# Kernel optimization log

Measured on AMD Instinct MI355X. Metric: run time of the kernel, lower is better.

## Reference

```python
import jax, jax.numpy as jnp
import numpy as np

N = 50000
E = 800000
D_IN = 128
D_HID = 128
D_OUT = 64


def setup_inputs() -> dict:
    key = jax.random.key(0)
    ks = jax.random.split(key, 9)
    x = jax.random.normal(ks[0], (N, D_IN), dtype=jnp.float32)
    edge_index = jax.random.randint(ks[1], (2, E), 0, N, dtype=jnp.int64)
    # PyG SAGEConv params: lin_l (neighbor path, with bias), lin_r (root path, no bias)
    s1 = 1.0 / np.sqrt(D_IN)
    s2 = 1.0 / np.sqrt(D_HID)
    return {
        "x": x,
        "edge_index": edge_index,
        "W1l": jax.random.uniform(ks[2], (D_IN, D_HID), jnp.float32, -s1, s1),
        "b1": jax.random.uniform(ks[3], (D_HID,), jnp.float32, -s1, s1),
        "W1r": jax.random.uniform(ks[4], (D_IN, D_HID), jnp.float32, -s1, s1),
        "W2l": jax.random.uniform(ks[5], (D_HID, D_OUT), jnp.float32, -s2, s2),
        "b2": jax.random.uniform(ks[6], (D_OUT,), jnp.float32, -s2, s2),
        "W2r": jax.random.uniform(ks[7], (D_HID, D_OUT), jnp.float32, -s2, s2),
    }


def _sage_conv(h, src, dst, Wl, b, Wr, n_nodes):
    # mean-aggregate source features onto target nodes
    msg = h[src]  # [E, d] gather
    summed = jax.ops.segment_sum(msg, dst, num_segments=n_nodes)
    cnt = jax.ops.segment_sum(jnp.ones((src.shape[0],), h.dtype), dst, num_segments=n_nodes)
    mean = summed / jnp.maximum(cnt, 1.0)[:, None]
    return mean @ Wl + b + h @ Wr


def reference(x, edge_index, W1l, b1, W1r, W2l, b2, W2r):
    src, dst = edge_index[0], edge_index[1]
    n = x.shape[0]
    h = jax.nn.relu(_sage_conv(x, src, dst, W1l, b1, W1r, n))
    # dropout is identity in eval mode
    return _sage_conv(h, src, dst, W2l, b2, W2r, n)
```

## Files before the change

kernel.cpp:

```cpp
#include <hip/hip_runtime.h>

#define NN   50000
#define NE   800000
#define CAP  48
#define NPG  6250
#define EPB  3125
#define SEG  576

#define BIN_BLOCKS  256
#define CVT_BLOCKS  (3125 + 128)
#define ZERO_BLOCKS 196
#define SCAT_BLOCKS 2048

typedef __attribute__((ext_vector_type(8))) short bf16x8;
typedef __attribute__((ext_vector_type(4))) unsigned short u16x4;
typedef __attribute__((ext_vector_type(4))) float f32x4;

__device__ __forceinline__ unsigned short f2b(float f) {
    unsigned int u = __builtin_bit_cast(unsigned int, f);
    u += 0x7FFFu + ((u >> 16) & 1u);
    return (unsigned short)(u >> 16);
}
__device__ __forceinline__ float b2f_lo(unsigned int u) {
    return __builtin_bit_cast(float, u << 16);
}
__device__ __forceinline__ float b2f_hi(unsigned int u) {
    return __builtin_bit_cast(float, u & 0xFFFF0000u);
}

__global__ __launch_bounds__(256) void prep_kernel(const int* __restrict__ src,
                                                   const int* __restrict__ dst,
                                                   int* __restrict__ bcnt,
                                                   unsigned* __restrict__ stage,
                                                   const float* __restrict__ x,
                                                   const float* __restrict__ W1l,
                                                   const float* __restrict__ W1r,
                                                   const float* __restrict__ W2l,
                                                   const float* __restrict__ W2r,
                                                   unsigned short* __restrict__ xb,
                                                   unsigned short* __restrict__ Bt1,
                                                   unsigned short* __restrict__ Bt2,
                                                   int* __restrict__ cursor) {
    if (blockIdx.x < BIN_BLOCKS) {
        __shared__ int cnt[16][8];
        __shared__ int repoff[16][8];
        const int tid = threadIdx.x;
        const int b   = blockIdx.x;
        const int r   = tid >> 4;
        if (tid < 128) ((int*)cnt)[tid] = 0;
        __syncthreads();

        unsigned recs[13], metas[13];
#pragma unroll
        for (int it = 0; it < 13; ++it) {
            const int i = it * 256 + tid;
            metas[it] = 0xFFFFFFFFu;
            if (i < EPB) {
                const int e = b * EPB + i;
                const int s = src[e], d = dst[e];
                const int g = d / NPG;
                const int dloc = d - g * NPG;
                const int slot = atomicAdd(&cnt[r][g], 1);
                recs[it]  = ((unsigned)dloc << 16) | (unsigned)s;
                metas[it] = ((unsigned)r << 20) | ((unsigned)g << 16) | (unsigned)slot;
            }
        }
        __syncthreads();
        if (tid < 8) {
            int off = 0;
#pragma unroll
            for (int rr = 0; rr < 16; ++rr) { repoff[rr][tid] = off; off += cnt[rr][tid]; }
            bcnt[tid * 256 + b] = off;
        }
        __syncthreads();
#pragma unroll
        for (int it = 0; it < 13; ++it) {
            if (metas[it] != 0xFFFFFFFFu) {
                const int rr   = metas[it] >> 20;
                const int g    = (metas[it] >> 16) & 7;
                const int slot = metas[it] & 0xFFFF;
                const int pos  = repoff[rr][g] + slot;
                if (pos < SEG) stage[((g << 8) + b) * SEG + pos] = recs[it];
            }
        }
    } else if (blockIdx.x < BIN_BLOCKS + 3125) {
        int i = (blockIdx.x - BIN_BLOCKS) * 256 + threadIdx.x;
        const float4* p = reinterpret_cast<const float4*>(x) + (size_t)i * 2;
        float4 a = p[0], b = p[1];
        uint4 u;
        u.x = (unsigned)f2b(a.x) | ((unsigned)f2b(a.y) << 16);
        u.y = (unsigned)f2b(a.z) | ((unsigned)f2b(a.w) << 16);
        u.z = (unsigned)f2b(b.x) | ((unsigned)f2b(b.y) << 16);
        u.w = (unsigned)f2b(b.z) | ((unsigned)f2b(b.w) << 16);
        reinterpret_cast<uint4*>(xb)[i] = u;
    } else if (blockIdx.x < BIN_BLOCKS + CVT_BLOCKS) {
        int t = (blockIdx.x - BIN_BLOCKS - 3125) * 256 + threadIdx.x;
        if (t < 32768) {
            int c = t >> 8, k = t & 255;
            float v = (k < 128) ? W1l[k * 128 + c] : W1r[(k - 128) * 128 + c];
            Bt1[c * 256 + k] = f2b(v);
        }
        if (t < 16384) {
            int c = t >> 7, k = t & 127;
            float v = (c < 64) ? W2l[k * 64 + c] : W2r[k * 64 + (c - 64)];
            Bt2[c * 128 + k] = f2b(v);
        }
    } else {
        int i = (blockIdx.x - BIN_BLOCKS - CVT_BLOCKS) * 256 + threadIdx.x;
        if (i < NN) cursor[i] = 0;
    }
}

__global__ __launch_bounds__(256) void scatter_kernel(const int* __restrict__ bcnt,
                                                      const unsigned* __restrict__ stage,
                                                      int* __restrict__ cursor,
                                                      unsigned short* __restrict__ col) {
    const int g = blockIdx.x & 7;
    const int b = blockIdx.x >> 3;
    int cnt = bcnt[g * 256 + b];
    if (cnt > SEG) cnt = SEG;
    const unsigned* sp = stage + (size_t)((g << 8) + b) * SEG;
    const int n0 = g * NPG;
    for (int i = threadIdx.x; i < cnt; i += 256) {
        unsigned rec = sp[i];
        int d = n0 + (int)(rec >> 16);
        int p = atomicAdd(&cursor[d], 1);
        if (p < CAP) col[d * CAP + p] = (unsigned short)(rec & 0xFFFFu);
    }
}

__global__ __launch_bounds__(256) void agg_gemm12(const unsigned short* __restrict__ xb,
                                                  const int* __restrict__ cursor,
                                                  const unsigned short* __restrict__ col,
                                                  const unsigned short* __restrict__ Bt1,
                                                  const unsigned short* __restrict__ Bt2,
                                                  const float* __restrict__ b1,
                                                  unsigned short* __restrict__ hlb,
                                                  unsigned short* __restrict__ hrb) {
    constexpr int LDA = 264;
    constexpr int LDH = 136;
    __shared__ unsigned short As[64 * LDA];

    const int base = blockIdx.x * 64;
    const int tid  = threadIdx.x;
    const int l    = tid & 15;
    const int sub  = tid >> 4;

    const uint4* fp = reinterpret_cast<const uint4*>(xb);

    for (int gq = 0; gq < 4; ++gq) {
        const int r  = gq * 16 + sub;
        const int gn = base + r;
        float a0 = 0.f, a1 = 0.f, a2 = 0.f, a3 = 0.f,
              a4 = 0.f, a5 = 0.f, a6 = 0.f, a7 = 0.f;
        uint4 xrow = make_uint4(0, 0, 0, 0);
        if (gn < NN) {
            int len = cursor[gn];
            len = (len > CAP) ? CAP : len;
            const unsigned short* cl = col + gn * CAP;
            int j = 0;
            for (; j + 4 <= len; j += 4) {
                u16x4 c4 = *reinterpret_cast<const u16x4*>(cl + j);
                uint4 v0 = fp[(int)c4[0] * 16 + l];
                uint4 v1 = fp[(int)c4[1] * 16 + l];
                uint4 v2 = fp[(int)c4[2] * 16 + l];
                uint4 v3 = fp[(int)c4[3] * 16 + l];
                a0 += (b2f_lo(v0.x) + b2f_lo(v1.x)) + (b2f_lo(v2.x) + b2f_lo(v3.x));
                a1 += (b2f_hi(v0.x) + b2f_hi(v1.x)) + (b2f_hi(v2.x) + b2f_hi(v3.x));
                a2 += (b2f_lo(v0.y) + b2f_lo(v1.y)) + (b2f_lo(v2.y) + b2f_lo(v3.y));
                a3 += (b2f_hi(v0.y) + b2f_hi(v1.y)) + (b2f_hi(v2.y) + b2f_hi(v3.y));
                a4 += (b2f_lo(v0.z) + b2f_lo(v1.z)) + (b2f_lo(v2.z) + b2f_lo(v3.z));
                a5 += (b2f_hi(v0.z) + b2f_hi(v1.z)) + (b2f_hi(v2.z) + b2f_hi(v3.z));
                a6 += (b2f_lo(v0.w) + b2f_lo(v1.w)) + (b2f_lo(v2.w) + b2f_lo(v3.w));
                a7 += (b2f_hi(v0.w) + b2f_hi(v1.w)) + (b2f_hi(v2.w) + b2f_hi(v3.w));
            }
            for (; j < len; ++j) {
                uint4 v0 = fp[(int)cl[j] * 16 + l];
                a0 += b2f_lo(v0.x);  a1 += b2f_hi(v0.x);
                a2 += b2f_lo(v0.y);  a3 += b2f_hi(v0.y);
                a4 += b2f_lo(v0.z);  a5 += b2f_hi(v0.z);
                a6 += b2f_lo(v0.w);  a7 += b2f_hi(v0.w);
            }
            const float inv = 1.0f / fmaxf((float)len, 1.0f);
            a0 *= inv; a1 *= inv; a2 *= inv; a3 *= inv;
            a4 *= inv; a5 *= inv; a6 *= inv; a7 *= inv;
            xrow = fp[gn * 16 + l];
        }
        uint4 u;
        u.x = (unsigned)f2b(a0) | ((unsigned)f2b(a1) << 16);
        u.y = (unsigned)f2b(a2) | ((unsigned)f2b(a3) << 16);
        u.z = (unsigned)f2b(a4) | ((unsigned)f2b(a5) << 16);
        u.w = (unsigned)f2b(a6) | ((unsigned)f2b(a7) << 16);
        *reinterpret_cast<uint4*>(&As[r * LDA + l * 8])       = u;
        *reinterpret_cast<uint4*>(&As[r * LDA + 128 + l * 8]) = xrow;
    }
    __syncthreads();

    const int wid  = tid >> 6, lane = tid & 63;
    const int lr   = lane & 15;
    const int lk   = (lane >> 4) * 8;
    const int ccol = lane & 15;
    const int ri   = (lane >> 4) * 4;

    f32x4 acc[4][2];
#pragma unroll
    for (int t = 0; t < 4; ++t) {
        acc[t][0] = (f32x4){0.f, 0.f, 0.f, 0.f};
        acc[t][1] = (f32x4){0.f, 0.f, 0.f, 0.f};
    }
    for (int ks = 0; ks < 8; ++ks) {
        const int k = ks * 32 + lk;
        bf16x8 b0 = *reinterpret_cast<const bf16x8*>(Bt1 + (size_t)(wid * 32 + lr) * 256 + k);
        bf16x8 b1 = *reinterpret_cast<const bf16x8*>(Bt1 + (size_t)(wid * 32 + 16 + lr) * 256 + k);
#pragma unroll
        for (int t = 0; t < 4; ++t) {
            bf16x8 a = *reinterpret_cast<const bf16x8*>(&As[(t * 16 + lr) * LDA + k]);
            acc[t][0] = __builtin_amdgcn_mfma_f32_16x16x32_bf16(a, b0, acc[t][0], 0, 0, 0);
            acc[t][1] = __builtin_amdgcn_mfma_f32_16x16x32_bf16(a, b1, acc[t][1], 0, 0, 0);
        }
    }
    __syncthreads();

    unsigned short* Hs = As;
#pragma unroll
    for (int t = 0; t < 4; ++t) {
#pragma unroll
        for (int f = 0; f < 2; ++f) {
            const int colg = wid * 32 + f * 16 + ccol;
            const float bv = b1[colg];
#pragma unroll
            for (int i = 0; i < 4; ++i) {
                Hs[(t * 16 + ri + i) * LDH + colg] = f2b(fmaxf(acc[t][f][i] + bv, 0.f));
            }
        }
    }
    __syncthreads();

    f32x4 acc2[4][2];
#pragma unroll
    for (int t = 0; t < 4; ++t) {
        acc2[t][0] = (f32x4){0.f, 0.f, 0.f, 0.f};
        acc2[t][1] = (f32x4){0.f, 0.f, 0.f, 0.f};
    }
    for (int ks = 0; ks < 4; ++ks) {
        const int k = ks * 32 + lk;
        bf16x8 b0 = *reinterpret_cast<const bf16x8*>(Bt2 + (size_t)(wid * 32 + lr) * 128 + k);
        bf16x8 b1 = *reinterpret_cast<const bf16x8*>(Bt2 + (size_t)(wid * 32 + 16 + lr) * 128 + k);
#pragma unroll
        for (int t = 0; t < 4; ++t) {
            bf16x8 a = *reinterpret_cast<const bf16x8*>(&Hs[(t * 16 + lr) * LDH + k]);
            acc2[t][0] = __builtin_amdgcn_mfma_f32_16x16x32_bf16(a, b0, acc2[t][0], 0, 0, 0);
            acc2[t][1] = __builtin_amdgcn_mfma_f32_16x16x32_bf16(a, b1, acc2[t][1], 0, 0, 0);
        }
    }

#pragma unroll
    for (int t = 0; t < 4; ++t) {
#pragma unroll
        for (int f = 0; f < 2; ++f) {
            const int colg = wid * 32 + f * 16 + ccol;
#pragma unroll
            for (int i = 0; i < 4; ++i) {
                const int gn = base + t * 16 + ri + i;
                if (gn < NN) {
                    float v = acc2[t][f][i];
                    if (colg < 64) hlb[(size_t)gn * 64 + colg] = f2b(v);
                    else           hrb[(size_t)gn * 64 + (colg - 64)] = f2b(v);
                }
            }
        }
    }
}

__global__ __launch_bounds__(256) void agg2_kernel(const unsigned short* __restrict__ feat,
                                                   const int* __restrict__ cursor,
                                                   const unsigned short* __restrict__ col,
                                                   const unsigned short* __restrict__ hrb,
                                                   const float* __restrict__ b2,
                                                   float* __restrict__ outf) {
    const int n = blockIdx.x * 32 + (threadIdx.x >> 3);
    const int l = threadIdx.x & 7;
    if (n >= NN) return;
    int len = cursor[n];
    len = (len > CAP) ? CAP : len;
    float a0 = 0.f, a1 = 0.f, a2 = 0.f, a3 = 0.f, a4 = 0.f, a5 = 0.f, a6 = 0.f, a7 = 0.f;
    const uint4* fp = reinterpret_cast<const uint4*>(feat);
    const unsigned short* cl = col + n * CAP;

    int j = 0;
    for (; j + 4 <= len; j += 4) {
        u16x4 c4 = *reinterpret_cast<const u16x4*>(cl + j);
        uint4 v0 = fp[(int)c4[0] * 8 + l];
        uint4 v1 = fp[(int)c4[1] * 8 + l];
        uint4 v2 = fp[(int)c4[2] * 8 + l];
        uint4 v3 = fp[(int)c4[3] * 8 + l];
        a0 += (b2f_lo(v0.x) + b2f_lo(v1.x)) + (b2f_lo(v2.x) + b2f_lo(v3.x));
        a1 += (b2f_hi(v0.x) + b2f_hi(v1.x)) + (b2f_hi(v2.x) + b2f_hi(v3.x));
        a2 += (b2f_lo(v0.y) + b2f_lo(v1.y)) + (b2f_lo(v2.y) + b2f_lo(v3.y));
        a3 += (b2f_hi(v0.y) + b2f_hi(v1.y)) + (b2f_hi(v2.y) + b2f_hi(v3.y));
        a4 += (b2f_lo(v0.z) + b2f_lo(v1.z)) + (b2f_lo(v2.z) + b2f_lo(v3.z));
        a5 += (b2f_hi(v0.z) + b2f_hi(v1.z)) + (b2f_hi(v2.z) + b2f_hi(v3.z));
        a6 += (b2f_lo(v0.w) + b2f_lo(v1.w)) + (b2f_lo(v2.w) + b2f_lo(v3.w));
        a7 += (b2f_hi(v0.w) + b2f_hi(v1.w)) + (b2f_hi(v2.w) + b2f_hi(v3.w));
    }
    for (; j < len; ++j) {
        uint4 v0 = fp[(int)cl[j] * 8 + l];
        a0 += b2f_lo(v0.x);  a1 += b2f_hi(v0.x);
        a2 += b2f_lo(v0.y);  a3 += b2f_hi(v0.y);
        a4 += b2f_lo(v0.z);  a5 += b2f_hi(v0.z);
        a6 += b2f_lo(v0.w);  a7 += b2f_hi(v0.w);
    }
    const float inv = 1.0f / fmaxf((float)len, 1.0f);
    uint4 hv = reinterpret_cast<const uint4*>(hrb)[(size_t)n * 8 + l];
    const float4* bp = reinterpret_cast<const float4*>(b2 + l * 8);
    float4 bv0 = bp[0], bv1 = bp[1];
    float4 o0 = make_float4(a0 * inv + b2f_lo(hv.x) + bv0.x,
                            a1 * inv + b2f_hi(hv.x) + bv0.y,
                            a2 * inv + b2f_lo(hv.y) + bv0.z,
                            a3 * inv + b2f_hi(hv.y) + bv0.w);
    float4 o1 = make_float4(a4 * inv + b2f_lo(hv.z) + bv1.x,
                            a5 * inv + b2f_hi(hv.z) + bv1.y,
                            a6 * inv + b2f_lo(hv.w) + bv1.z,
                            a7 * inv + b2f_hi(hv.w) + bv1.w);
    float4* op = reinterpret_cast<float4*>(outf + (size_t)n * 64) + l * 2;
    op[0] = o0; op[1] = o1;
}

extern "C" void kernel_launch(void* const* d_in, const int* in_sizes, int n_in,
                              void* d_out, int out_size, void* d_ws, size_t ws_size,
                              hipStream_t stream) {
    const float* x   = (const float*)d_in[0];
    const int*   ei  = (const int*)d_in[1];
    const float* W1l = (const float*)d_in[2];
    const float* b1  = (const float*)d_in[3];
    const float* W1r = (const float*)d_in[4];
    const float* W2l = (const float*)d_in[5];
    const float* b2  = (const float*)d_in[6];
    const float* W2r = (const float*)d_in[7];

    const int* src = ei;
    const int* dst = ei + NE;

    char* ws = (char*)d_ws;
    int* cursor = (int*)ws;
    int* bcnt   = (int*)(ws + 200000);
    unsigned short* col = (unsigned short*)(ws + 208384);
    unsigned short* xb  = (unsigned short*)(ws + 9808384);
    unsigned short* hlb = (unsigned short*)(ws + 22608384);
    unsigned short* hrb = (unsigned short*)(ws + 29008384);
    unsigned*       stage = (unsigned*)(ws + 35408384);
    unsigned short* Bt1 = (unsigned short*)(ws + 48208384);
    unsigned short* Bt2 = (unsigned short*)(ws + 48273920);
    float* outp = (float*)d_out;

    prep_kernel<<<BIN_BLOCKS + CVT_BLOCKS + ZERO_BLOCKS, 256, 0, stream>>>(
        src, dst, bcnt, stage, x, W1l, W1r, W2l, W2r, xb, Bt1, Bt2, cursor);
    scatter_kernel<<<SCAT_BLOCKS, 256, 0, stream>>>(bcnt, stage, cursor, col);

    agg_gemm12<<<(NN + 63) / 64, 256, 0, stream>>>(xb, cursor, col, Bt1, Bt2,
                                                   b1, hlb, hrb);

    agg2_kernel<<<(NN + 31) / 32, 256, 0, stream>>>(hlb, cursor, col, hrb, b2, outp);
}
```

Before: 115.0 us.

## Store layer-2 neighbor features in FP8 e4m3 and interleave blocks across node groups

The layer-2 neighbor-path projection (hl) is now stored as a custom 8-bit e4m3-style encoding instead of bf16, which halves the bytes gathered per edge in the second aggregation kernel. The decode adds integer ops per element. Block indices are also remapped so consecutive blocks cover different node groups of size NPG, which spreads work across graph partitions and may help cache locality. The custom encoding has no denormals or saturation handling and cuts precision, so accuracy risk rises.

```diff
diff --git a/kernel.cpp b/kernel.cpp
--- a/kernel.cpp
+++ b/kernel.cpp
@@ -26,6 +26,16 @@
 }
 __device__ __forceinline__ float b2f_hi(unsigned int u) {
     return __builtin_bit_cast(float, u & 0xFFFF0000u);
+}
+__device__ __forceinline__ unsigned e4m3_enc(float f) {
+    float g = f * 0x1p-120f;
+    unsigned u = __builtin_bit_cast(unsigned, g);
+    u += 0x7FFFFu + ((u >> 20) & 1u);
+    return ((u >> 20) & 0x7Fu) | ((u >> 24) & 0x80u);
+}
+__device__ __forceinline__ float e4m3_dec(unsigned b) {
+    unsigned bits = ((b & 0x80u) << 24) | ((b & 0x7Fu) << 20);
+    return __builtin_bit_cast(float, bits) * 0x1p120f;
 }
 
 __global__ __launch_bounds__(256) void prep_kernel(const int* __restrict__ src,
@@ -135,26 +145,28 @@
                                                   const unsigned short* __restrict__ Bt1,
                                                   const unsigned short* __restrict__ Bt2,
                                                   const float* __restrict__ b1,
-                                                  unsigned short* __restrict__ hlb,
+                                                  unsigned char* __restrict__ hl8,
                                                   unsigned short* __restrict__ hrb) {
     constexpr int LDA = 264;
     constexpr int LDH = 136;
     __shared__ unsigned short As[64 * LDA];
 
-    const int base = blockIdx.x * 64;
-    const int tid  = threadIdx.x;
-    const int l    = tid & 15;
-    const int sub  = tid >> 4;
+    const int g     = blockIdx.x & 7;
+    const int lbase = (blockIdx.x >> 3) * 64;
+    const int gbase = g * NPG + lbase;
+    const int tid   = threadIdx.x;
+    const int l     = tid & 15;
+    const int sub   = tid >> 4;
 
     const uint4* fp = reinterpret_cast<const uint4*>(xb);
 
     for (int gq = 0; gq < 4; ++gq) {
         const int r  = gq * 16 + sub;
-        const int gn = base + r;
+        const int gn = gbase + r;
         float a0 = 0.f, a1 = 0.f, a2 = 0.f, a3 = 0.f,
               a4 = 0.f, a5 = 0.f, a6 = 0.f, a7 = 0.f;
         uint4 xrow = make_uint4(0, 0, 0, 0);
-        if (gn < NN) {
+        if (lbase + r < NPG) {
             int len = cursor[gn];
             len = (len > CAP) ? CAP : len;
             const unsigned short* cl = col + gn * CAP;
@@ -261,10 +273,11 @@
             const int colg = wid * 32 + f * 16 + ccol;
 #pragma unroll
             for (int i = 0; i < 4; ++i) {
-                const int gn = base + t * 16 + ri + i;
-                if (gn < NN) {
+                const int lrow = lbase + t * 16 + ri + i;
+                if (lrow < NPG) {
+                    const int gn = g * NPG + lrow;
                     float v = acc2[t][f][i];
-                    if (colg < 64) hlb[(size_t)gn * 64 + colg] = f2b(v);
+                    if (colg < 64) hl8[(size_t)gn * 64 + colg] = (unsigned char)e4m3_enc(v);
                     else           hrb[(size_t)gn * 64 + (colg - 64)] = f2b(v);
                 }
             }
@@ -272,43 +285,53 @@
     }
 }
 
-__global__ __launch_bounds__(256) void agg2_kernel(const unsigned short* __restrict__ feat,
+__global__ __launch_bounds__(256) void agg2_kernel(const unsigned char* __restrict__ hl8,
                                                    const int* __restrict__ cursor,
                                                    const unsigned short* __restrict__ col,
                                                    const unsigned short* __restrict__ hrb,
                                                    const float* __restrict__ b2,
                                                    float* __restrict__ outf) {
-    const int n = blockIdx.x * 32 + (threadIdx.x >> 3);
-    const int l = threadIdx.x & 7;
-    if (n >= NN) return;
+    const int g    = blockIdx.x & 7;
+    const int lrow = (blockIdx.x >> 3) * 32 + (threadIdx.x >> 3);
+    const int l    = threadIdx.x & 7;
+    if (lrow >= NPG) return;
+    const int n = g * NPG + lrow;
     int len = cursor[n];
     len = (len > CAP) ? CAP : len;
     float a0 = 0.f, a1 = 0.f, a2 = 0.f, a3 = 0.f, a4 = 0.f, a5 = 0.f, a6 = 0.f, a7 = 0.f;
-    const uint4* fp = reinterpret_cast<const uint4*>(feat);
+    const uint2* fp = reinterpret_cast<const uint2*>(hl8);
     const unsigned short* cl = col + n * CAP;
 
     int j = 0;
     for (; j + 4 <= len; j += 4) {
         u16x4 c4 = *reinterpret_cast<const u16x4*>(cl + j);
-        uint4 v0 = fp[(int)c4[0] * 8 + l];
-        uint4 v1 = fp[(int)c4[1] * 8 + l];
-        uint4 v2 = fp[(int)c4[2] * 8 + l];
-        uint4 v3 = fp[(int)c4[3] * 8 + l];
-        a0 += (b2f_lo(v0.x) + b2f_lo(v1.x)) + (b2f_lo(v2.x) + b2f_lo(v3.x));
-        a1 += (b2f_hi(v0.x) + b2f_hi(v1.x)) + (b2f_hi(v2.x) + b2f_hi(v3.x));
-        a2 += (b2f_lo(v0.y) + b2f_lo(v1.y)) + (b2f_lo(v2.y) + b2f_lo(v3.y));
-        a3 += (b2f_hi(v0.y) + b2f_hi(v1.y)) + (b2f_hi(v2.y) + b2f_hi(v3.y));
-        a4 += (b2f_lo(v0.z) + b2f_lo(v1.z)) + (b2f_lo(v2.z) + b2f_lo(v3.z));
-        a5 += (b2f_hi(v0.z) + b2f_hi(v1.z)) + (b2f_hi(v2.z) + b2f_hi(v3.z));
-        a6 += (b2f_lo(v0.w) + b2f_lo(v1.w)) + (b2f_lo(v2.w) + b2f_lo(v3.w));
-        a7 += (b2f_hi(v0.w) + b2f_hi(v1.w)) + (b2f_hi(v2.w) + b2f_hi(v3.w));
+        uint2 v0 = fp[(int)c4[0] * 8 + l];
+        uint2 v1 = fp[(int)c4[1] * 8 + l];
+        uint2 v2 = fp[(int)c4[2] * 8 + l];
+        uint2 v3 = fp[(int)c4[3] * 8 + l];
+        a0 += (e4m3_dec(v0.x & 0xFF) + e4m3_dec(v1.x & 0xFF))
+            + (e4m3_dec(v2.x & 0xFF) + e4m3_dec(v3.x & 0xFF));
+        a1 += (e4m3_dec((v0.x >> 8) & 0xFF) + e4m3_dec((v1.x >> 8) & 0xFF))
+            + (e4m3_dec((v2.x >> 8) & 0xFF) + e4m3_dec((v3.x >> 8) & 0xFF));
+        a2 += (e4m3_dec((v0.x >> 16) & 0xFF) + e4m3_dec((v1.x >> 16) & 0xFF))
+            + (e4m3_dec((v2.x >> 16) & 0xFF) + e4m3_dec((v3.x >> 16) & 0xFF));
+        a3 += (e4m3_dec(v0.x >> 24) + e4m3_dec(v1.x >> 24))
+            + (e4m3_dec(v2.x >> 24) + e4m3_dec(v3.x >> 24));
+        a4 += (e4m3_dec(v0.y & 0xFF) + e4m3_dec(v1.y & 0xFF))
+            + (e4m3_dec(v2.y & 0xFF) + e4m3_dec(v3.y & 0xFF));
+        a5 += (e4m3_dec((v0.y >> 8) & 0xFF) + e4m3_dec((v1.y >> 8) & 0xFF))
+            + (e4m3_dec((v2.y >> 8) & 0xFF) + e4m3_dec((v3.y >> 8) & 0xFF));
+        a6 += (e4m3_dec((v0.y >> 16) & 0xFF) + e4m3_dec((v1.y >> 16) & 0xFF))
+            + (e4m3_dec((v2.y >> 16) & 0xFF) + e4m3_dec((v3.y >> 16) & 0xFF));
+        a7 += (e4m3_dec(v0.y >> 24) + e4m3_dec(v1.y >> 24))
+            + (e4m3_dec(v2.y >> 24) + e4m3_dec(v3.y >> 24));
     }
     for (; j < len; ++j) {
-        uint4 v0 = fp[(int)cl[j] * 8 + l];
-        a0 += b2f_lo(v0.x);  a1 += b2f_hi(v0.x);
-        a2 += b2f_lo(v0.y);  a3 += b2f_hi(v0.y);
-        a4 += b2f_lo(v0.z);  a5 += b2f_hi(v0.z);
-        a6 += b2f_lo(v0.w);  a7 += b2f_hi(v0.w);
+        uint2 v0 = fp[(int)cl[j] * 8 + l];
+        a0 += e4m3_dec(v0.x & 0xFF);         a1 += e4m3_dec((v0.x >> 8) & 0xFF);
+        a2 += e4m3_dec((v0.x >> 16) & 0xFF); a3 += e4m3_dec(v0.x >> 24);
+        a4 += e4m3_dec(v0.y & 0xFF);         a5 += e4m3_dec((v0.y >> 8) & 0xFF);
+        a6 += e4m3_dec((v0.y >> 16) & 0xFF); a7 += e4m3_dec(v0.y >> 24);
     }
     const float inv = 1.0f / fmaxf((float)len, 1.0f);
     uint4 hv = reinterpret_cast<const uint4*>(hrb)[(size_t)n * 8 + l];
@@ -346,7 +369,7 @@
     int* bcnt   = (int*)(ws + 200000);
     unsigned short* col = (unsigned short*)(ws + 208384);
     unsigned short* xb  = (unsigned short*)(ws + 9808384);
-    unsigned short* hlb = (unsigned short*)(ws + 22608384);
+    unsigned char*  hl8 = (unsigned char*)(ws + 22608384);
     unsigned short* hrb = (unsigned short*)(ws + 29008384);
     unsigned*       stage = (unsigned*)(ws + 35408384);
     unsigned short* Bt1 = (unsigned short*)(ws + 48208384);
@@ -357,8 +380,7 @@
         src, dst, bcnt, stage, x, W1l, W1r, W2l, W2r, xb, Bt1, Bt2, cursor);
     scatter_kernel<<<SCAT_BLOCKS, 256, 0, stream>>>(bcnt, stage, cursor, col);
 
-    agg_gemm12<<<(NN + 63) / 64, 256, 0, stream>>>(xb, cursor, col, Bt1, Bt2,
-                                                   b1, hlb, hrb);
-
-    agg2_kernel<<<(NN + 31) / 32, 256, 0, stream>>>(hlb, cursor, col, hrb, b2, outp);
-}
+    agg_gemm12<<<8 * 98, 256, 0, stream>>>(xb, cursor, col, Bt1, Bt2, b1, hl8, hrb);
+
+    agg2_kernel<<<8 * 196, 256, 0, stream>>>(hl8, cursor, col, hrb, b2, outp);
+}
```

Measured after the change: 120.5 us. 1.05x slower.
